# Kernel tuning notes

Measured on AMD Instinct MI355X. Metric: run time of the kernel, lower is better.

## Reference

```python
import jax, jax.numpy as jnp
import numpy as np

NE, NN, D, H, DH = 2048, 4096, 256, 8, 64
HD = H * DH
MAX_REL = 10


def setup_inputs() -> dict:
    key = jax.random.key(0)
    ks = jax.random.split(key, 10)
    inp = {}
    inp["hyperedge_features"] = jax.random.normal(ks[0], (NE, D), jnp.float32)
    inp["node_features"] = jax.random.normal(ks[1], (NN, D), jnp.float32)
    inp["incidence_matrix"] = jax.random.randint(ks[2], (NN, NE), 0, 2, jnp.int32)
    inp["node_types"] = jax.random.randint(ks[3], (NN,), 0, 2, jnp.int32)
    he_idx = jax.random.randint(ks[4], (NE,), 0, 4, jnp.int32)
    inp["hyperedge_types"] = jnp.array([0, 2, 3, 4], jnp.int32)[he_idx]  # valid query types
    s = 1.0 / np.sqrt(D)
    # per-type projection tables; query types indexed 0..4 (slot 1 unused, matches ModuleDict keys {0,2,3,4})
    inp["Wq"] = jax.random.normal(ks[5], (5, D, HD), jnp.float32) * s
    inp["Wk"] = jax.random.normal(ks[6], (2, D, HD), jnp.float32) * s
    inp["Wv"] = jax.random.normal(ks[7], (2, D, HD), jnp.float32) * s
    inp["Wo"] = jax.random.normal(ks[8], (HD + D, D), jnp.float32) * (1.0 / np.sqrt(HD + D))
    inp["bo"] = jnp.zeros((D,), jnp.float32)
    inp["gamma_e"] = jnp.ones((D,), jnp.float32)
    inp["beta_e"] = jnp.zeros((D,), jnp.float32)
    inp["gamma_n"] = jnp.ones((D,), jnp.float32)
    inp["beta_n"] = jnp.zeros((D,), jnp.float32)
    inp["rel_emb"] = jax.random.normal(ks[9], (2 * MAX_REL + 1, H), jnp.float32) * 0.02
    return inp


def _ln(x, g, b, eps=1e-5):
    m = jnp.mean(x, axis=-1, keepdims=True)
    v = jnp.var(x, axis=-1, keepdims=True)
    return (x - m) * jax.lax.rsqrt(v + eps) * g + b


def reference(hyperedge_features, node_features, incidence_matrix, node_types,
              hyperedge_types, Wq, Wk, Wv, Wo, bo, gamma_e, beta_e, gamma_n,
              beta_n, rel_emb):
    scale = DH ** 0.5
    e = _ln(hyperedge_features, gamma_e, beta_e)  # [NE, D]
    x = _ln(node_features, gamma_n, beta_n)       # [NN, D]
    # type-conditioned projections: project with every type table, gather per token
    q = jnp.einsum('nd,tdk->tnk', e, Wq)[hyperedge_types, jnp.arange(NE)]  # [NE, HD]
    k = jnp.einsum('nd,tdk->tnk', x, Wk)[node_types, jnp.arange(NN)]      # [NN, HD]
    v = jnp.einsum('nd,tdk->tnk', x, Wv)[node_types, jnp.arange(NN)]
    # 'n (h d) -> h n d'
    q = q.reshape(NE, H, DH).transpose(1, 0, 2)
    k = k.reshape(NN, H, DH).transpose(1, 0, 2)
    v = v.reshape(NN, H, DH).transpose(1, 0, 2)
    scores = jnp.einsum('hid,hjd->hij', q, k) / scale  # [H, NE, NN]
    mask = (incidence_matrix.T == 0)[None]             # [1, NE, NN]
    scores = jnp.where(mask, -jnp.inf, scores)
    rel = jnp.clip(jnp.arange(NE)[:, None] - jnp.arange(NN)[None, :], -MAX_REL, MAX_REL) + MAX_REL
    scores = scores + rel_emb[rel].transpose(2, 0, 1)  # pos bias added after mask, as in torch
    w = jax.nn.softmax(scores, axis=-1)                # dropout is identity in eval
    out = jnp.einsum('hij,hjd->hid', w, v)
    out = out.transpose(1, 0, 2).reshape(NE, HD)       # 'h n d -> n (h d)'
    out = jax.nn.silu(out)
    final = jnp.concatenate([e, out], axis=-1) @ Wo + bo
    return final, scores
```

## Files before the change

### kernel.cpp

```cpp
#include <hip/hip_runtime.h>
#include <cmath>

#define NE 2048
#define NN 4096
#define D 256
#define H 8
#define DH 64
#define HD 512
#define MAXREL 10
#define NREL 21
#define NEG_BIG -3.0e38f
#define L2E 1.44269504f

typedef __attribute__((ext_vector_type(8))) short bf16x8;
typedef __attribute__((ext_vector_type(4))) float f32x4;

__device__ inline short f2bf(float x) {
  union { float f; unsigned u; } c; c.f = x;
  unsigned r = (c.u + 0x7FFFu + ((c.u >> 16) & 1u)) >> 16;
  return (short)r;
}
__device__ inline short f2bf_t(float x) {
  return (short)(__float_as_uint(x) >> 16);
}

__device__ inline void gl_lds16(const void* g, void* l) {
  __builtin_amdgcn_global_load_lds(
      (const __attribute__((address_space(1))) void*)g,
      (__attribute__((address_space(3))) void*)l, 16, 0, 0);
}

__global__ __launch_bounds__(256) void prep_all(
    const float* __restrict__ he, const int* __restrict__ htyp,
    const float* __restrict__ ge, const float* __restrict__ be,
    const float* __restrict__ nf, const int* __restrict__ ntyp,
    const float* __restrict__ gn, const float* __restrict__ bn,
    const int* __restrict__ inc, const float* __restrict__ Wq,
    const float* __restrict__ Wk, const float* __restrict__ Wv,
    float* __restrict__ e_ws, short* __restrict__ E2,
    short* __restrict__ X2, unsigned short* __restrict__ maskb,
    short* __restrict__ Wqf, short* __restrict__ Wkf,
    short* __restrict__ Wvf) {
  const int bid = blockIdx.x;
  const int t = threadIdx.x;
  __shared__ float part[4];
  __shared__ float bc[2];
  __shared__ float lnv[D];

  if (bid < NE) {
    const int i = bid;
    const float x = he[(size_t)i * D + t];
    float s = x;
#pragma unroll
    for (int off = 32; off > 0; off >>= 1) s += __shfl_down(s, off);
    if ((t & 63) == 0) part[t >> 6] = s;
    __syncthreads();
    if (t == 0) bc[0] = (part[0] + part[1] + part[2] + part[3]) * (1.0f / D);
    __syncthreads();
    const float mean = bc[0];
    const float dev = x - mean;
    float sq = dev * dev;
#pragma unroll
    for (int off = 32; off > 0; off >>= 1) sq += __shfl_down(sq, off);
    __syncthreads();
    if ((t & 63) == 0) part[t >> 6] = sq;
    __syncthreads();
    if (t == 0) bc[1] = (part[0] + part[1] + part[2] + part[3]) * (1.0f / D);
    __syncthreads();
    const float inv = rsqrtf(bc[1] + 1e-5f);
    const float v = dev * inv * ge[t] + be[t];
    lnv[t] = v;
    e_ws[(size_t)i * D + t] = v;
    __syncthreads();
    const int ht = htyp[i];
    const int slot = (ht == 0) ? 0 : ht - 1;
    const int iin = i & 15, rt = i >> 4;
    const int dd0 = 4 * t;
    const int kt = dd0 >> 5;
    const int lane = ((dd0 >> 2) & 3) * 16 + iin;
    const int e0 = ((dd0 >> 4) & 1) * 4;
    short v4[4];
#pragma unroll
    for (int u = 0; u < 4; ++u)
      v4[u] = ((dd0 >> 8) == slot) ? f2bf(lnv[(dd0 + u) & 255]) : (short)0;
    short* dst = E2 + ((size_t)(rt * 32 + kt) * 64 + lane) * 8 + e0;
    *(short4*)dst = make_short4(v4[0], v4[1], v4[2], v4[3]);
  } else if (bid < NE + NN) {
    const int j = bid - NE;
    const float x = nf[(size_t)j * D + t];
    float s = x;
#pragma unroll
    for (int off = 32; off > 0; off >>= 1) s += __shfl_down(s, off);
    if ((t & 63) == 0) part[t >> 6] = s;
    __syncthreads();
    if (t == 0) bc[0] = (part[0] + part[1] + part[2] + part[3]) * (1.0f / D);
    __syncthreads();
    const float mean = bc[0];
    const float dev = x - mean;
    float sq = dev * dev;
#pragma unroll
    for (int off = 32; off > 0; off >>= 1) sq += __shfl_down(sq, off);
    __syncthreads();
    if ((t & 63) == 0) part[t >> 6] = sq;
    __syncthreads();
    if (t == 0) bc[1] = (part[0] + part[1] + part[2] + part[3]) * (1.0f / D);
    __syncthreads();
    const float inv = rsqrtf(bc[1] + 1e-5f);
    lnv[t] = dev * inv * gn[t] + bn[t];
    __syncthreads();
    const int nt = ntyp[j];
    const int jin = j & 15, rt = j >> 4;
    const int dd0 = 2 * t;
    const int kt = dd0 >> 5;
    const int lane = ((dd0 >> 2) & 3) * 16 + jin;
    const int e0 = ((dd0 >> 4) & 1) * 4 + (dd0 & 3);
    const short v0 = ((dd0 >> 8) == nt) ? f2bf(lnv[dd0 & 255]) : (short)0;
    const short v1 = ((dd0 >> 8) == nt) ? f2bf(lnv[(dd0 + 1) & 255]) : (short)0;
    short* dst = X2 + ((size_t)(rt * 16 + kt) * 64 + lane) * 8 + e0;
    *(short2*)dst = make_short2(v0, v1);
  } else if (bid < NE + NN + NN / 2) {
    const int bb = bid - (NE + NN);
    const int it = t & 127;
    const int gj = bb * 2 + (t >> 7);
    const int* p = inc + (size_t)gj * NE + it * 16;
    unsigned m = 0;
#pragma unroll
    for (int r = 0; r < 16; ++r) m |= (p[r] != 0 ? 1u : 0u) << r;
    maskb[(size_t)it * NN + gj] = (unsigned short)m;
  } else if (bid < NE + NN + NN / 2 + 256) {
    const int bb = bid - (NE + NN + NN / 2);
    const int f = bb * 4 + (t >> 6);
    const int lane = t & 63;
    const int ct = f >> 5, kt = f & 31;
    const int c = ct * 16 + (lane & 15);
    const int khi = (lane >> 4) * 4;
    bf16x8 r;
#pragma unroll
    for (int e = 0; e < 8; ++e) {
      const int kk = (e >> 2) * 16 + khi + (e & 3);
      const int dd = kt * 32 + kk;
      const int sslot = dd >> 8;
      const int tt = (sslot == 0) ? 0 : sslot + 1;
      r[e] = f2bf(Wq[((size_t)tt * 256 + (dd & 255)) * 512 + c]);
    }
    *(bf16x8*)(Wqf + ((size_t)f * 64 + lane) * 8) = r;
  } else {
    const int bb = bid - (NE + NN + NN / 2 + 256);
    const int f = bb * 4 + (t >> 6);
    const int lane = t & 63;
    const int ct = f >> 4, kt = f & 15;
    const int c = ct * 16 + (lane & 15);
    const int khi = (lane >> 4) * 4;
    bf16x8 rk, rv;
#pragma unroll
    for (int e = 0; e < 8; ++e) {
      const int kk = (e >> 2) * 16 + khi + (e & 3);
      const int dd = kt * 32 + kk;
      rk[e] = f2bf(Wk[(size_t)dd * 512 + c]);
      rv[e] = f2bf(Wv[(size_t)dd * 512 + c]);
    }
    *(bf16x8*)(Wkf + ((size_t)f * 64 + lane) * 8) = rk;
    *(bf16x8*)(Wvf + ((size_t)f * 64 + lane) * 8) = rv;
  }
}

__global__ __launch_bounds__(256) void proj_all(
    const short* __restrict__ E2, const short* __restrict__ Wqf,
    short* __restrict__ Qp, const short* __restrict__ X2,
    const short* __restrict__ Wkf, const short* __restrict__ Wvf,
    short* __restrict__ Kp, short* __restrict__ Vp) {
  const int tid = threadIdx.x;
  const int w = tid >> 6, lane = tid & 63;
  __shared__ __align__(16) short tiles[2][12 * 512];

  if (blockIdx.x < 512) {
    const int RT0 = (blockIdx.x & 63) * 2;
    const int CT0 = (blockIdx.x >> 6) * 4;

#define QSTAGE(buf, ks)                                                        \
  do {                                                                         \
    const int rtl_ = w >> 1, ktl_ = w & 1;                                     \
    gl_lds16(E2 + ((size_t)((RT0 + rtl_) * 32 + (ks) * 2 + ktl_) * 64 + lane) * 8, \
             &tiles[buf][w * 512 + lane * 8]);                                 \
    gl_lds16(Wqf + ((size_t)((CT0 + (w >> 1)) * 32 + (ks) * 2 + (w & 1)) * 64 + lane) * 8, \
             &tiles[buf][(4 + w) * 512 + lane * 8]);                           \
    gl_lds16(Wqf + ((size_t)((CT0 + 2 + (w >> 1)) * 32 + (ks) * 2 + (w & 1)) * 64 + lane) * 8, \
             &tiles[buf][(8 + w) * 512 + lane * 8]);                           \
  } while (0)

    const int itl = w >> 1, ctp = w & 1;
    f32x4 acc[2] = {{0.f, 0.f, 0.f, 0.f}, {0.f, 0.f, 0.f, 0.f}};

    QSTAGE(0, 0);
    for (int ks = 0; ks < 16; ++ks) {
      const int cb = ks & 1;
      if (ks + 1 < 16) {
        QSTAGE(cb ^ 1, ks + 1);
        asm volatile("s_waitcnt vmcnt(3)" ::: "memory");
      } else {
        asm volatile("s_waitcnt vmcnt(0)" ::: "memory");
      }
      __builtin_amdgcn_s_barrier();
#pragma unroll
      for (int ktl = 0; ktl < 2; ++ktl) {
        const bf16x8 ef = *(const bf16x8*)&tiles[cb][(itl * 2 + ktl) * 512 + lane * 8];
#pragma unroll
        for (int ci = 0; ci < 2; ++ci) {
          const int ctl = ctp * 2 + ci;
          const bf16x8 qw = *(const bf16x8*)&tiles[cb][(4 + ctl * 2 + ktl) * 512 + lane * 8];
          acc[ci] = __builtin_amdgcn_mfma_f32_16x16x32_bf16(qw, ef, acc[ci], 0, 0, 0);
        }
      }
      __builtin_amdgcn_s_barrier();
    }

    const int it_g = RT0 + itl;
    const int ct_even = CT0 + ctp * 2;
    const int hh = ct_even >> 2, kc = (ct_even >> 1) & 1;
    bf16x8 fr;
#pragma unroll
    for (int r = 0; r < 4; ++r) { fr[r] = f2bf(acc[0][r]); fr[4 + r] = f2bf(acc[1][r]); }
    *(bf16x8*)(Qp + (((size_t)hh * (NE / 16) + it_g) * 2 + kc) * 512 + (size_t)lane * 8) = fr;
  } else {
    const int bb = blockIdx.x - 512;
    const int RT0 = (bb & 63) * 4;
    const int CT0 = (bb >> 6) * 4;

#define KVSTAGE(buf, kt)                                                       \
  do {                                                                         \
    gl_lds16(X2 + ((size_t)((RT0 + w) * 16 + (kt)) * 64 + lane) * 8,           \
             &tiles[buf][w * 512 + lane * 8]);                                 \
    gl_lds16(Wkf + ((size_t)((CT0 + w) * 16 + (kt)) * 64 + lane) * 8,          \
             &tiles[buf][(4 + w) * 512 + lane * 8]);                           \
    gl_lds16(Wvf + ((size_t)((CT0 + w) * 16 + (kt)) * 64 + lane) * 8,          \
             &tiles[buf][(8 + w) * 512 + lane * 8]);                           \
  } while (0)

    const int wr = w >> 1, wc = w & 1;
    f32x4 accK[2][2], accV[2][2];
#pragma unroll
    for (int a = 0; a < 2; ++a)
#pragma unroll
      for (int b = 0; b < 2; ++b) {
        accK[a][b] = (f32x4){0.f, 0.f, 0.f, 0.f};
        accV[a][b] = (f32x4){0.f, 0.f, 0.f, 0.f};
      }

    KVSTAGE(0, 0);
    for (int kt = 0; kt < 16; ++kt) {
      const int cb = kt & 1;
      if (kt + 1 < 16) {
        KVSTAGE(cb ^ 1, kt + 1);
        asm volatile("s_waitcnt vmcnt(3)" ::: "memory");
      } else {
        asm volatile("s_waitcnt vmcnt(0)" ::: "memory");
      }
      __builtin_amdgcn_s_barrier();
      bf16x8 xf[2], kf[2], vf[2];
#pragma unroll
      for (int p = 0; p < 2; ++p) {
        xf[p] = *(const bf16x8*)&tiles[cb][(wr * 2 + p) * 512 + lane * 8];
        kf[p] = *(const bf16x8*)&tiles[cb][(4 + wc * 2 + p) * 512 + lane * 8];
        vf[p] = *(const bf16x8*)&tiles[cb][(8 + wc * 2 + p) * 512 + lane * 8];
      }
#pragma unroll
      for (int ci = 0; ci < 2; ++ci)
#pragma unroll
        for (int ji = 0; ji < 2; ++ji) {
          accK[ci][ji] = __builtin_amdgcn_mfma_f32_16x16x32_bf16(kf[ci], xf[ji], accK[ci][ji], 0, 0, 0);
          accV[ji][ci] = __builtin_amdgcn_mfma_f32_16x16x32_bf16(xf[ji], vf[ci], accV[ji][ci], 0, 0, 0);
        }
      __builtin_amdgcn_s_barrier();
    }

    const int ct_even = CT0 + wc * 2;
    const int hh = ct_even >> 2, kc = (ct_even >> 1) & 1;
#pragma unroll
    for (int ji = 0; ji < 2; ++ji) {
      const int jt16 = RT0 + wr * 2 + ji;
      bf16x8 fr;
#pragma unroll
      for (int r = 0; r < 4; ++r) { fr[r] = f2bf(accK[0][ji][r]); fr[4 + r] = f2bf(accK[1][ji][r]); }
      *(bf16x8*)(Kp + (((((size_t)hh * 64 + (jt16 >> 2)) * 4 + (jt16 & 3)) * 2 + kc) * 512) + (size_t)lane * 8) = fr;
    }
    const int jt_even = RT0 + wr * 2;
    const int jt64 = jt_even >> 2, kcv = (jt_even >> 1) & 1;
#pragma unroll
    for (int ci = 0; ci < 2; ++ci) {
      const int ctg = CT0 + wc * 2 + ci;
      const int hhv = ctg >> 2, dh16 = ctg & 3;
      bf16x8 fr;
#pragma unroll
      for (int r = 0; r < 4; ++r) { fr[r] = f2bf(accV[0][ci][r]); fr[4 + r] = f2bf(accV[1][ci][r]); }
      *(bf16x8*)(Vp + ((((size_t)hhv * 64 + jt64) * 4 + dh16) * 2 + kcv) * 512 + (size_t)lane * 8) = fr;
    }
  }
}

__global__ __launch_bounds__(256) void attn_mfma(
    const short* __restrict__ Qp, const short* __restrict__ Kp,
    const short* __restrict__ Vp, const unsigned short* __restrict__ maskb,
    const float* __restrict__ rel_emb, float* __restrict__ scores,
    float* __restrict__ po, float* __restrict__ pm, float* __restrict__ pl,
    int tps) {
  const int h = blockIdx.y;
  const int split = blockIdx.z;
  const int tid = threadIdx.x;
  const int wid = tid >> 6;
  const int lane = tid & 63;
  const int i0w = blockIdx.x * 64 + wid * 16;
  const int gi = i0w + (lane & 15);
  const int gi15 = lane & 15;
  const int lhi4 = (lane >> 4) * 4;
  const int jt0 = split * tps;
  const int itw = i0w >> 4;

  __shared__ __align__(16) short Kt[2][4096];
  __shared__ __align__(16) short Vt[2][4096];
  __shared__ __align__(16) unsigned short Ms[4][2][64];
  __shared__ float relb[NREL];

  if (tid < NREL) relb[tid] = rel_emb[tid * H + h];
  __syncthreads();

  const size_t qbase = (((size_t)h * (NE / 16) + (i0w >> 4)) * 2) * 512 + (size_t)lane * 8;
  const bf16x8 qf0 = *(const bf16x8*)(Qp + qbase);
  const bf16x8 qf1 = *(const bf16x8*)(Qp + qbase + 512);

  const short* kgh = Kp + (size_t)h * 64 * 4096;
  const short* vgh = Vp + (size_t)h * 64 * 4096;
  const unsigned short* mgh = maskb + (size_t)itw * NN;

#define STAGE(buf, jt)                                              \
  do {                                                              \
    const short* kg_ = kgh + (size_t)(jt) * 4096 + tid * 8;         \
    const short* vg_ = vgh + (size_t)(jt) * 4096 + tid * 8;         \
    gl_lds16(kg_, &Kt[buf][tid * 8]);                               \
    gl_lds16(kg_ + 2048, &Kt[buf][2048 + tid * 8]);                 \
    gl_lds16(vg_, &Vt[buf][tid * 8]);                               \
    gl_lds16(vg_ + 2048, &Vt[buf][2048 + tid * 8]);                 \
    if (lane < 8)                                                   \
      gl_lds16(mgh + (size_t)(jt) * 64 + lane * 8,                  \
               &Ms[wid][buf][lane * 8]);                            \
  } while (0)

  STAGE(0, jt0);
  asm volatile("s_waitcnt vmcnt(0)" ::: "memory");
  __builtin_amdgcn_s_barrier();

  float m_run = -INFINITY, l_run = 0.f;
  f32x4 o0 = {0.f, 0.f, 0.f, 0.f}, o1 = o0, o2 = o0, o3 = o0;

  for (int t = 0; t < tps; ++t) {
    const int jb = jt0 + t;
    const int b = t & 1;
    if (t + 1 < tps) {
      STAGE(b ^ 1, jb + 1);
      if (t > 0) { asm volatile("s_waitcnt vmcnt(9)" ::: "memory"); }
    } else {
      if (t > 0) { asm volatile("s_waitcnt vmcnt(4)" ::: "memory"); }
    }
    __builtin_amdgcn_s_barrier();

    const int j0 = jb * 64;
    const float bc0 = relb[0], bc20 = relb[20];
    const bool allhi = (j0 > i0w + 15 + MAXREL);
    const bool alllo = (j0 + 63 < i0w - MAXREL);

    float lg[4][4];
#pragma unroll
    for (int ms = 0; ms < 4; ++ms) {
      const bf16x8 ka = *(const bf16x8*)&Kt[b][(ms * 2 + 0) * 512 + lane * 8];
      const bf16x8 kb = *(const bf16x8*)&Kt[b][(ms * 2 + 1) * 512 + lane * 8];
      f32x4 sf = {0.f, 0.f, 0.f, 0.f};
      __builtin_amdgcn_s_setprio(1);
      sf = __builtin_amdgcn_mfma_f32_16x16x32_bf16(ka, qf0, sf, 0, 0, 0);
      sf = __builtin_amdgcn_mfma_f32_16x16x32_bf16(kb, qf1, sf, 0, 0, 0);
      __builtin_amdgcn_s_setprio(0);
      const int jb0 = j0 + ms * 16 + lhi4;
      const uint2 mw = *(const uint2*)&Ms[wid][b][ms * 16 + lhi4];
#pragma unroll
      for (int r = 0; r < 4; ++r) {
        const int gj = jb0 + r;
        float bias;
        if (allhi) bias = bc0;
        else if (alllo) bias = bc20;
        else {
          int dd = gi - gj;
          dd = dd < -MAXREL ? -MAXREL : (dd > MAXREL ? MAXREL : dd);
          bias = relb[dd + MAXREL];
        }
        const unsigned word = (r < 2) ? mw.x : mw.y;
        const unsigned ok = (word >> ((r & 1) * 16 + gi15)) & 1u;
        lg[ms][r] = ok ? fmaf(sf[r], 0.125f, bias) : -INFINITY;
      }
      f32x4 sv;
      sv[0] = fmaxf(lg[ms][0], NEG_BIG);
      sv[1] = fmaxf(lg[ms][1], NEG_BIG);
      sv[2] = fmaxf(lg[ms][2], NEG_BIG);
      sv[3] = fmaxf(lg[ms][3], NEG_BIG);
      __builtin_nontemporal_store(sv,
          (f32x4*)(scores + ((size_t)h * NE + gi) * NN + jb0));
    }

    float tmax = -INFINITY;
#pragma unroll
    for (int ms = 0; ms < 4; ++ms)
#pragma unroll
      for (int r = 0; r < 4; ++r) tmax = fmaxf(tmax, lg[ms][r]);
    tmax = fmaxf(tmax, __shfl_xor(tmax, 16));
    tmax = fmaxf(tmax, __shfl_xor(tmax, 32));
    const float mnew = fmaxf(m_run, tmax);
    const float rs = (m_run == mnew) ? 1.f : exp2f((m_run - mnew) * L2E);
    float p[4][4];
    float ps = 0.f;
#pragma unroll
    for (int ms = 0; ms < 4; ++ms)
#pragma unroll
      for (int r = 0; r < 4; ++r) {
        const float v = lg[ms][r];
        const float pe = (v == -INFINITY) ? 0.f : exp2f((v - mnew) * L2E);
        p[ms][r] = pe;
        ps += pe;
      }
    l_run = l_run * rs + ps;
    m_run = mnew;
    if (!__all(rs == 1.0f)) { o0 *= rs; o1 *= rs; o2 *= rs; o3 *= rs; }

    bf16x8 pb0, pb1;
    pb0[0] = f2bf_t(p[0][0]); pb0[1] = f2bf_t(p[0][1]); pb0[2] = f2bf_t(p[0][2]); pb0[3] = f2bf_t(p[0][3]);
    pb0[4] = f2bf_t(p[1][0]); pb0[5] = f2bf_t(p[1][1]); pb0[6] = f2bf_t(p[1][2]); pb0[7] = f2bf_t(p[1][3]);
    pb1[0] = f2bf_t(p[2][0]); pb1[1] = f2bf_t(p[2][1]); pb1[2] = f2bf_t(p[2][2]); pb1[3] = f2bf_t(p[2][3]);
    pb1[4] = f2bf_t(p[3][0]); pb1[5] = f2bf_t(p[3][1]); pb1[6] = f2bf_t(p[3][2]); pb1[7] = f2bf_t(p[3][3]);

    __builtin_amdgcn_s_setprio(1);
    o0 = __builtin_amdgcn_mfma_f32_16x16x32_bf16(*(const bf16x8*)&Vt[b][0 * 512 + lane * 8], pb0, o0, 0, 0, 0);
    o0 = __builtin_amdgcn_mfma_f32_16x16x32_bf16(*(const bf16x8*)&Vt[b][1 * 512 + lane * 8], pb1, o0, 0, 0, 0);
    o1 = __builtin_amdgcn_mfma_f32_16x16x32_bf16(*(const bf16x8*)&Vt[b][2 * 512 + lane * 8], pb0, o1, 0, 0, 0);
    o1 = __builtin_amdgcn_mfma_f32_16x16x32_bf16(*(const bf16x8*)&Vt[b][3 * 512 + lane * 8], pb1, o1, 0, 0, 0);
    o2 = __builtin_amdgcn_mfma_f32_16x16x32_bf16(*(const bf16x8*)&Vt[b][4 * 512 + lane * 8], pb0, o2, 0, 0, 0);
    o2 = __builtin_amdgcn_mfma_f32_16x16x32_bf16(*(const bf16x8*)&Vt[b][5 * 512 + lane * 8], pb1, o2, 0, 0, 0);
    o3 = __builtin_amdgcn_mfma_f32_16x16x32_bf16(*(const bf16x8*)&Vt[b][6 * 512 + lane * 8], pb0, o3, 0, 0, 0);
    o3 = __builtin_amdgcn_mfma_f32_16x16x32_bf16(*(const bf16x8*)&Vt[b][7 * 512 + lane * 8], pb1, o3, 0, 0, 0);
    __builtin_amdgcn_s_setprio(0);

    asm volatile("s_waitcnt lgkmcnt(0)" ::: "memory");
    __builtin_amdgcn_s_barrier();
  }

  l_run += __shfl_xor(l_run, 16);
  l_run += __shfl_xor(l_run, 32);
  const size_t pbase = ((size_t)split * H + h) * NE + gi;
  if (lane < 16) { pm[pbase] = m_run; pl[pbase] = l_run; }
  float* pob = po + pbase * DH + lhi4;
  *(float4*)(pob +  0) = make_float4(o0[0], o0[1], o0[2], o0[3]);
  *(float4*)(pob + 16) = make_float4(o1[0], o1[1], o1[2], o1[3]);
  *(float4*)(pob + 32) = make_float4(o2[0], o2[1], o2[2], o2[3]);
  *(float4*)(pob + 48) = make_float4(o3[0], o3[1], o3[2], o3[3]);
}

__global__ __launch_bounds__(256) void combine_kernel(
    const float* __restrict__ po, const float* __restrict__ pm,
    const float* __restrict__ pl, float* __restrict__ aout, int splits) {
  const int g = blockIdx.x * 4 + (threadIdx.x >> 6);
  const int dh = threadIdx.x & 63;
  const int h = g >> 11;
  const int i = g & (NE - 1);
  float M = -INFINITY;
  for (int s = 0; s < splits; ++s)
    M = fmaxf(M, pm[((size_t)s * H + h) * NE + i]);
  float L = 0.f, o = 0.f;
  for (int s = 0; s < splits; ++s) {
    const size_t pb = ((size_t)s * H + h) * NE + i;
    const float ms = pm[pb];
    if (ms > -INFINITY) {
      const float wgt = exp2f((ms - M) * L2E);
      L += wgt * pl[pb];
      o += wgt * po[pb * DH + dh];
    }
  }
  const float a = o / L;
  aout[(size_t)i * HD + h * DH + dh] = a / (1.f + expf(-a));
}

__global__ __launch_bounds__(256) void final_kernel(
    const float* __restrict__ e, const float* __restrict__ att,
    const float* __restrict__ Wo, const float* __restrict__ bo,
    float* __restrict__ out) {
  const int r0 = blockIdx.x * 4;
  const int tid = threadIdx.x;
  __shared__ float rows[4][HD + D];
  for (int u = tid; u < 4 * (HD + D); u += 256) {
    const int r = u / (HD + D);
    const int c = u - r * (HD + D);
    rows[r][c] = (c < D) ? e[(size_t)(r0 + r) * D + c]
                         : att[(size_t)(r0 + r) * HD + (c - D)];
  }
  __syncthreads();
  float acc[4] = {0, 0, 0, 0};
  for (int dd = 0; dd < HD + D; ++dd) {
    const float w = Wo[(size_t)dd * D + tid];
#pragma unroll
    for (int r = 0; r < 4; ++r) acc[r] += rows[r][dd] * w;
  }
  const float b = bo[tid];
#pragma unroll
  for (int r = 0; r < 4; ++r) out[(size_t)(r0 + r) * D + tid] = acc[r] + b;
}

extern "C" void kernel_launch(void* const* d_in, const int* in_sizes, int n_in,
                              void* d_out, int out_size, void* d_ws, size_t ws_size,
                              hipStream_t stream) {
  (void)in_sizes; (void)n_in; (void)out_size;
  const float* he   = (const float*)d_in[0];
  const float* nf   = (const float*)d_in[1];
  const int*   inc  = (const int*)d_in[2];
  const int*   ntyp = (const int*)d_in[3];
  const int*   htyp = (const int*)d_in[4];
  const float* Wq   = (const float*)d_in[5];
  const float* Wk   = (const float*)d_in[6];
  const float* Wv   = (const float*)d_in[7];
  const float* Wo   = (const float*)d_in[8];
  const float* bo   = (const float*)d_in[9];
  const float* ge   = (const float*)d_in[10];
  const float* be   = (const float*)d_in[11];
  const float* gn   = (const float*)d_in[12];
  const float* bn   = (const float*)d_in[13];
  const float* rel  = (const float*)d_in[14];

  float* outf = (float*)d_out;
  float* outs = outf + (size_t)NE * D;

  float* e_ws = (float*)d_ws;
  float* a_ws = e_ws + (size_t)NE * D;
  short* X2   = (short*)(a_ws + (size_t)NE * HD);
  short* E2   = X2 + (size_t)NN * 512;
  short* Wkf  = E2 + (size_t)NE * 1024;
  short* Wvf  = Wkf + (size_t)512 * 512;
  short* Wqf  = Wvf + (size_t)512 * 512;
  short* Qp   = Wqf + (size_t)512 * 1024;
  short* Kp   = Qp + (size_t)NE * HD;
  short* Vp   = Kp + (size_t)NN * HD;
  unsigned short* maskb = (unsigned short*)(Vp + (size_t)NN * HD);
  float* po   = (float*)(maskb + (size_t)(NE / 16) * NN);

  const size_t base_f = (size_t)(po - e_ws);
  int splits = 8;
  while (splits > 1 &&
         (base_f + (size_t)splits * H * NE * (DH + 2)) * 4 > ws_size)
    splits >>= 1;
  float* pm = po + (size_t)splits * H * NE * DH;
  float* pl = pm + (size_t)splits * H * NE;
  const int tps = NN / 64 / splits;

  prep_all<<<NE + NN + NN / 2 + 256 + 128, 256, 0, stream>>>(
      he, htyp, ge, be, nf, ntyp, gn, bn, inc, Wq, Wk, Wv,
      e_ws, E2, X2, maskb, Wqf, Wkf, Wvf);
  proj_all<<<1024, 256, 0, stream>>>(E2, Wqf, Qp, X2, Wkf, Wvf, Kp, Vp);
  attn_mfma<<<dim3(NE / 64, H, splits), 256, 0, stream>>>(
      Qp, Kp, Vp, maskb, rel, outs, po, pm, pl, tps);
  combine_kernel<<<NE * H / 4, 256, 0, stream>>>(po, pm, pl, a_ws, splits);
  final_kernel<<<NE / 4, 256, 0, stream>>>(e_ws, a_ws, Wo, bo, outf);
}
```

Before: 188.4 us.

## Run final output projection on bf16 MFMA with fragment-packed inputs

Replaces the scalar fp32 final projection with an MFMA bf16 GEMM. prep_all now writes the layer-normed hyperedge features and a pre-packed bf16 copy of Wo straight into MFMA fragment layout. The combine kernel writes SiLU outputs into that same packed buffer instead of an fp32 workspace. The default split count for the attention partials also drops from 8 to 4, which reduces combine traffic but gives the attention kernel fewer blocks. The cost is bf16 rounding in the final GEMM inputs.

```diff
diff --git a/kernel.cpp b/kernel.cpp
--- a/kernel.cpp
+++ b/kernel.cpp
@@ -37,10 +37,11 @@
     const float* __restrict__ gn, const float* __restrict__ bn,
     const int* __restrict__ inc, const float* __restrict__ Wq,
     const float* __restrict__ Wk, const float* __restrict__ Wv,
-    float* __restrict__ e_ws, short* __restrict__ E2,
-    short* __restrict__ X2, unsigned short* __restrict__ maskb,
-    short* __restrict__ Wqf, short* __restrict__ Wkf,
-    short* __restrict__ Wvf) {
+    const float* __restrict__ Wo,
+    short* __restrict__ E2, short* __restrict__ X2,
+    unsigned short* __restrict__ maskb, short* __restrict__ Wqf,
+    short* __restrict__ Wkf, short* __restrict__ Wvf,
+    short* __restrict__ Rf, short* __restrict__ Wof) {
   const int bid = blockIdx.x;
   const int t = threadIdx.x;
   __shared__ float part[4];
@@ -70,21 +71,30 @@
     const float inv = rsqrtf(bc[1] + 1e-5f);
     const float v = dev * inv * ge[t] + be[t];
     lnv[t] = v;
-    e_ws[(size_t)i * D + t] = v;
     __syncthreads();
     const int ht = htyp[i];
     const int slot = (ht == 0) ? 0 : ht - 1;
     const int iin = i & 15, rt = i >> 4;
-    const int dd0 = 4 * t;
-    const int kt = dd0 >> 5;
-    const int lane = ((dd0 >> 2) & 3) * 16 + iin;
-    const int e0 = ((dd0 >> 4) & 1) * 4;
-    short v4[4];
-#pragma unroll
-    for (int u = 0; u < 4; ++u)
-      v4[u] = ((dd0 >> 8) == slot) ? f2bf(lnv[(dd0 + u) & 255]) : (short)0;
-    short* dst = E2 + ((size_t)(rt * 32 + kt) * 64 + lane) * 8 + e0;
-    *(short4*)dst = make_short4(v4[0], v4[1], v4[2], v4[3]);
+    {
+      const int dd0 = 4 * t;
+      const int kt = dd0 >> 5;
+      const int lane = ((dd0 >> 2) & 3) * 16 + iin;
+      const int e0 = ((dd0 >> 4) & 1) * 4;
+      short v4[4];
+#pragma unroll
+      for (int u = 0; u < 4; ++u)
+        v4[u] = ((dd0 >> 8) == slot) ? f2bf(lnv[(dd0 + u) & 255]) : (short)0;
+      short* dst = E2 + ((size_t)(rt * 32 + kt) * 64 + lane) * 8 + e0;
+      *(short4*)dst = make_short4(v4[0], v4[1], v4[2], v4[3]);
+    }
+    if (t < 128) {
+      const int c0 = 2 * t;
+      const int kt = c0 >> 5, kk = c0 & 31;
+      const int l = ((kk >> 2) & 3) * 16 + iin;
+      const int ee = (kk >> 4) * 4 + (kk & 3);
+      short* dst = Rf + ((size_t)(rt * 24 + kt) * 64 + l) * 8 + ee;
+      *(short2*)dst = make_short2(f2bf(lnv[c0]), f2bf(lnv[c0 + 1]));
+    }
   } else if (bid < NE + NN) {
     const int j = bid - NE;
     const float x = nf[(size_t)j * D + t];
@@ -144,7 +154,7 @@
       r[e] = f2bf(Wq[((size_t)tt * 256 + (dd & 255)) * 512 + c]);
     }
     *(bf16x8*)(Wqf + ((size_t)f * 64 + lane) * 8) = r;
-  } else {
+  } else if (bid < NE + NN + NN / 2 + 256 + 128) {
     const int bb = bid - (NE + NN + NN / 2 + 256);
     const int f = bb * 4 + (t >> 6);
     const int lane = t & 63;
@@ -161,6 +171,21 @@
     }
     *(bf16x8*)(Wkf + ((size_t)f * 64 + lane) * 8) = rk;
     *(bf16x8*)(Wvf + ((size_t)f * 64 + lane) * 8) = rv;
+  } else {
+    const int bb = bid - (NE + NN + NN / 2 + 256 + 128);
+    const int f = bb * 4 + (t >> 6);
+    const int lane = t & 63;
+    const int ct = f / 24, kt = f - ct * 24;
+    const int c = ct * 16 + (lane & 15);
+    const int khi = (lane >> 4) * 4;
+    bf16x8 r;
+#pragma unroll
+    for (int e = 0; e < 8; ++e) {
+      const int kk = (e >> 2) * 16 + khi + (e & 3);
+      const int dd = kt * 32 + kk;
+      r[e] = f2bf(Wo[(size_t)dd * 256 + c]);
+    }
+    *(bf16x8*)(Wof + ((size_t)f * 64 + lane) * 8) = r;
   }
 }
 
@@ -461,51 +486,94 @@
 
 __global__ __launch_bounds__(256) void combine_kernel(
     const float* __restrict__ po, const float* __restrict__ pm,
-    const float* __restrict__ pl, float* __restrict__ aout, int splits) {
-  const int g = blockIdx.x * 4 + (threadIdx.x >> 6);
-  const int dh = threadIdx.x & 63;
+    const float* __restrict__ pl, short* __restrict__ Rf, int splits) {
+  const int g = blockIdx.x * 8 + (threadIdx.x >> 5);
+  const int dh0 = (threadIdx.x & 31) * 2;
   const int h = g >> 11;
   const int i = g & (NE - 1);
   float M = -INFINITY;
   for (int s = 0; s < splits; ++s)
     M = fmaxf(M, pm[((size_t)s * H + h) * NE + i]);
-  float L = 0.f, o = 0.f;
+  float L = 0.f, o0 = 0.f, o1 = 0.f;
   for (int s = 0; s < splits; ++s) {
     const size_t pb = ((size_t)s * H + h) * NE + i;
     const float ms = pm[pb];
     if (ms > -INFINITY) {
       const float wgt = exp2f((ms - M) * L2E);
       L += wgt * pl[pb];
-      o += wgt * po[pb * DH + dh];
+      o0 += wgt * po[pb * DH + dh0];
+      o1 += wgt * po[pb * DH + dh0 + 1];
     }
   }
-  const float a = o / L;
-  aout[(size_t)i * HD + h * DH + dh] = a / (1.f + expf(-a));
-}
-
-__global__ __launch_bounds__(256) void final_kernel(
-    const float* __restrict__ e, const float* __restrict__ att,
-    const float* __restrict__ Wo, const float* __restrict__ bo,
-    float* __restrict__ out) {
-  const int r0 = blockIdx.x * 4;
+  const float a0 = o0 / L, a1 = o1 / L;
+  const float s0 = a0 / (1.f + expf(-a0));
+  const float s1 = a1 / (1.f + expf(-a1));
+  const int col = 256 + h * DH + dh0;
+  const int kt = col >> 5, kk = col & 31;
+  const int l = ((kk >> 2) & 3) * 16 + (i & 15);
+  const int ee = (kk >> 4) * 4 + (kk & 3);
+  short* dst = Rf + ((size_t)((i >> 4) * 24 + kt) * 64 + l) * 8 + ee;
+  *(short2*)dst = make_short2(f2bf(s0), f2bf(s1));
+}
+
+__global__ __launch_bounds__(256) void final_mfma(
+    const short* __restrict__ Rf, const short* __restrict__ Wof,
+    const float* __restrict__ bo, float* __restrict__ out) {
   const int tid = threadIdx.x;
-  __shared__ float rows[4][HD + D];
-  for (int u = tid; u < 4 * (HD + D); u += 256) {
-    const int r = u / (HD + D);
-    const int c = u - r * (HD + D);
-    rows[r][c] = (c < D) ? e[(size_t)(r0 + r) * D + c]
-                         : att[(size_t)(r0 + r) * HD + (c - D)];
+  const int w = tid >> 6, lane = tid & 63;
+  const int RT0 = blockIdx.x * 2;
+  const int CT0 = blockIdx.y * 4;
+  __shared__ __align__(16) short tiles[2][12 * 512];
+
+#define FSTAGE(buf, ks)                                                        \
+  do {                                                                         \
+    const int rtl_ = w >> 1, ktl_ = w & 1;                                     \
+    gl_lds16(Rf + ((size_t)((RT0 + rtl_) * 24 + (ks) * 2 + ktl_) * 64 + lane) * 8, \
+             &tiles[buf][w * 512 + lane * 8]);                                 \
+    gl_lds16(Wof + ((size_t)((CT0 + (w >> 1)) * 24 + (ks) * 2 + (w & 1)) * 64 + lane) * 8, \
+             &tiles[buf][(4 + w) * 512 + lane * 8]);                           \
+    gl_lds16(Wof + ((size_t)((CT0 + 2 + (w >> 1)) * 24 + (ks) * 2 + (w & 1)) * 64 + lane) * 8, \
+             &tiles[buf][(8 + w) * 512 + lane * 8]);                           \
+  } while (0)
+
+  const int itl = w >> 1, ctp = w & 1;
+  f32x4 acc[2] = {{0.f, 0.f, 0.f, 0.f}, {0.f, 0.f, 0.f, 0.f}};
+
+  FSTAGE(0, 0);
+  for (int ks = 0; ks < 12; ++ks) {
+    const int cb = ks & 1;
+    if (ks + 1 < 12) {
+      FSTAGE(cb ^ 1, ks + 1);
+      asm volatile("s_waitcnt vmcnt(3)" ::: "memory");
+    } else {
+      asm volatile("s_waitcnt vmcnt(0)" ::: "memory");
+    }
+    __builtin_amdgcn_s_barrier();
+#pragma unroll
+    for (int ktl = 0; ktl < 2; ++ktl) {
+      const bf16x8 rf = *(const bf16x8*)&tiles[cb][(itl * 2 + ktl) * 512 + lane * 8];
+#pragma unroll
+      for (int ci = 0; ci < 2; ++ci) {
+        const int ctl = ctp * 2 + ci;
+        const bf16x8 wf = *(const bf16x8*)&tiles[cb][(4 + ctl * 2 + ktl) * 512 + lane * 8];
+        acc[ci] = __builtin_amdgcn_mfma_f32_16x16x32_bf16(wf, rf, acc[ci], 0, 0, 0);
+      }
+    }
+    __builtin_amdgcn_s_barrier();
   }
-  __syncthreads();
-  float acc[4] = {0, 0, 0, 0};
-  for (int dd = 0; dd < HD + D; ++dd) {
-    const float w = Wo[(size_t)dd * D + tid];
-#pragma unroll
-    for (int r = 0; r < 4; ++r) acc[r] += rows[r][dd] * w;
+
+  const int gi = (RT0 + itl) * 16 + (lane & 15);
+  const int lhi4 = (lane >> 4) * 4;
+#pragma unroll
+  for (int ci = 0; ci < 2; ++ci) {
+    const int c0 = (CT0 + ctp * 2 + ci) * 16 + lhi4;
+    float4 o;
+    o.x = acc[ci][0] + bo[c0];
+    o.y = acc[ci][1] + bo[c0 + 1];
+    o.z = acc[ci][2] + bo[c0 + 2];
+    o.w = acc[ci][3] + bo[c0 + 3];
+    *(float4*)(out + (size_t)gi * D + c0) = o;
   }
-  const float b = bo[tid];
-#pragma unroll
-  for (int r = 0; r < 4; ++r) out[(size_t)(r0 + r) * D + tid] = acc[r] + b;
 }
 
 extern "C" void kernel_launch(void* const* d_in, const int* in_sizes, int n_in,
@@ -531,9 +599,7 @@
   float* outf = (float*)d_out;
   float* outs = outf + (size_t)NE * D;
 
-  float* e_ws = (float*)d_ws;
-  float* a_ws = e_ws + (size_t)NE * D;
-  short* X2   = (short*)(a_ws + (size_t)NE * HD);
+  short* X2   = (short*)d_ws;
   short* E2   = X2 + (size_t)NN * 512;
   short* Wkf  = E2 + (size_t)NE * 1024;
   short* Wvf  = Wkf + (size_t)512 * 512;
@@ -541,24 +607,26 @@
   short* Qp   = Wqf + (size_t)512 * 1024;
   short* Kp   = Qp + (size_t)NE * HD;
   short* Vp   = Kp + (size_t)NN * HD;
-  unsigned short* maskb = (unsigned short*)(Vp + (size_t)NN * HD);
+  short* Rf   = Vp + (size_t)NN * HD;
+  short* Wof  = Rf + (size_t)128 * 24 * 512;
+  unsigned short* maskb = (unsigned short*)(Wof + (size_t)384 * 512);
   float* po   = (float*)(maskb + (size_t)(NE / 16) * NN);
 
-  const size_t base_f = (size_t)(po - e_ws);
-  int splits = 8;
+  const size_t used_bytes = (size_t)((char*)po - (char*)d_ws);
+  int splits = 4;
   while (splits > 1 &&
-         (base_f + (size_t)splits * H * NE * (DH + 2)) * 4 > ws_size)
+         used_bytes + (size_t)splits * H * NE * (DH + 2) * 4 > ws_size)
     splits >>= 1;
   float* pm = po + (size_t)splits * H * NE * DH;
   float* pl = pm + (size_t)splits * H * NE;
   const int tps = NN / 64 / splits;
 
-  prep_all<<<NE + NN + NN / 2 + 256 + 128, 256, 0, stream>>>(
-      he, htyp, ge, be, nf, ntyp, gn, bn, inc, Wq, Wk, Wv,
-      e_ws, E2, X2, maskb, Wqf, Wkf, Wvf);
+  prep_all<<<NE + NN + NN / 2 + 256 + 128 + 96, 256, 0, stream>>>(
+      he, htyp, ge, be, nf, ntyp, gn, bn, inc, Wq, Wk, Wv, Wo,
+      E2, X2, maskb, Wqf, Wkf, Wvf, Rf, Wof);
   proj_all<<<1024, 256, 0, stream>>>(E2, Wqf, Qp, X2, Wkf, Wvf, Kp, Vp);
   attn_mfma<<<dim3(NE / 64, H, splits), 256, 0, stream>>>(
       Qp, Kp, Vp, maskb, rel, outs, po, pm, pl, tps);
-  combine_kernel<<<NE * H / 4, 256, 0, stream>>>(po, pm, pl, a_ws, splits);
-  final_kernel<<<NE / 4, 256, 0, stream>>>(e_ws, a_ws, Wo, bo, outf);
-}
+  combine_kernel<<<NE * H / 8, 256, 0, stream>>>(po, pm, pl, Rf, splits);
+  final_mfma<<<dim3(64, 4), 256, 0, stream>>>(Rf, Wof, bo, outf);
+}
```

Result: slower. 194.0 us (+3.0%).
